# Optimization experiments

Hardware: AMD Instinct MI355X
Metric: run time of the kernel (lower is better)

Reference implementation:

```python
import jax, jax.numpy as jnp
import numpy as np

MODEL_DIM = 1024
NUM_HEADS = 16
HEAD_DIM = MODEL_DIM // NUM_HEADS
B, T = 4, 2048


def setup_inputs() -> dict:
    key = jax.random.key(0)
    ks = jax.random.split(key, 11)
    s = 1.0 / np.sqrt(MODEL_DIM)  # torch Linear default-ish init scale
    def lin(kw, kb):
        W = jax.random.uniform(kw, (MODEL_DIM, MODEL_DIM), jnp.float32, -s, s)
        b = jax.random.uniform(kb, (MODEL_DIM,), jnp.float32, -s, s)
        return W, b
    Wq, bq = lin(ks[0], ks[1])
    Wk, bk = lin(ks[2], ks[3])
    Wv, bv = lin(ks[4], ks[5])
    Wo, bo = lin(ks[6], ks[7])
    query = jax.random.normal(ks[8], (B, T, MODEL_DIM), jnp.float32)
    key_t = jax.random.normal(ks[9], (B, T, MODEL_DIM), jnp.float32)
    value = jax.random.normal(ks[10], (B, T, MODEL_DIM), jnp.float32)
    return {"query": query, "key": key_t, "value": value,
            "Wq": Wq, "bq": bq, "Wk": Wk, "bk": bk,
            "Wv": Wv, "bv": bv, "Wo": Wo, "bo": bo}


def reference(query, key, value, Wq, bq, Wk, bk, Wv, bv, Wo, bo):
    b, tq, d = query.shape
    tk = key.shape[-2]
    h, hd = NUM_HEADS, HEAD_DIM
    # projections; split last dim into heads (torch split/cat == reshape to [b,t,h,hd])
    q = (query @ Wq.T + bq).reshape(b, tq, h, hd)
    k = (key @ Wk.T + bk).reshape(b, tk, h, hd)
    v = (value @ Wv.T + bv).reshape(b, tk, h, hd)
    score = jnp.einsum('bqhd,bkhd->bhqk', q, k) / np.sqrt(hd).astype(np.float32)
    causal = jnp.tril(jnp.ones((tq, tk), dtype=bool))  # mask=True path
    score = jnp.where(causal, score, -jnp.inf)
    probs = jax.nn.softmax(score, axis=-1)
    out = jnp.einsum('bhqk,bkhd->bqhd', probs, v).reshape(b, tq, d)
    return out @ Wo.T + bo
```

## Files before the change

### kernel.cpp

```cpp
#include <hip/hip_runtime.h>
#include <stdint.h>

#define T_SEQ 2048
#define NB    4
#define NH    16
#define DH    64
#define DM    1024
#define MTOT  (NB * T_SEQ)

typedef __attribute__((ext_vector_type(8)))  short  short8;
typedef __attribute__((ext_vector_type(8)))  __bf16 bf16x8;
typedef __attribute__((ext_vector_type(4)))  float  f32x4;
typedef __attribute__((ext_vector_type(16))) float  f32x16;
typedef __attribute__((ext_vector_type(4)))  unsigned short ushort4v;
typedef __attribute__((ext_vector_type(4)))  unsigned int   uint4v;
typedef unsigned short ushort;
typedef unsigned long long u64;

__device__ __forceinline__ ushort f2bf(float x) {
    unsigned int u = __builtin_bit_cast(unsigned int, x);
    u += 0x7FFFu + ((u >> 16) & 1u);
    return (ushort)(u >> 16);
}

__device__ __forceinline__ unsigned cvtpk(float lo, float hi) {
    unsigned r;
    asm("v_cvt_pk_bf16_f32 %0, %1, %2" : "=v"(r) : "v"(lo), "v"(hi));
    return r;
}

__device__ __forceinline__ f32x4 mfma16(short8 a, short8 b, f32x4 c) {
    return __builtin_amdgcn_mfma_f32_16x16x32_bf16(
        __builtin_bit_cast(bf16x8, a), __builtin_bit_cast(bf16x8, b), c, 0, 0, 0);
}
__device__ __forceinline__ f32x16 mfma32(short8 a, short8 b, f32x16 c) {
    return __builtin_amdgcn_mfma_f32_32x32x16_bf16(
        __builtin_bit_cast(bf16x8, a), __builtin_bit_cast(bf16x8, b), c, 0, 0, 0);
}

#define GLOBAL_AS(p) ((const __attribute__((address_space(1))) void*)(p))
#define LDS_AS(p)    ((__attribute__((address_space(3))) void*)(p))

__global__ void cvt4_kernel(const float* __restrict__ s0, const float* __restrict__ s1,
                            const float* __restrict__ s2, const float* __restrict__ s3,
                            ushort* __restrict__ dst) {
    int i = blockIdx.x * 256 + threadIdx.x;
    int which = i >> 18;
    int loc   = i & 262143;
    const float* s = which == 0 ? s0 : which == 1 ? s1 : which == 2 ? s2 : s3;
    f32x4 v = ((const f32x4*)s)[loc];
    ushort4v r;
    r[0] = f2bf(v[0]); r[1] = f2bf(v[1]); r[2] = f2bf(v[2]); r[3] = f2bf(v[3]);
    ((ushort4v*)dst)[i] = r;
}

__global__ __launch_bounds__(256, 4)
void proj_gemm(const float* __restrict__ Xq, const float* __restrict__ Xk,
               const float* __restrict__ Xv, const ushort* __restrict__ Wall,
               const float* __restrict__ bq, const float* __restrict__ bk,
               const float* __restrict__ bv, ushort* __restrict__ P0,
               ushort* __restrict__ Vt, float qscale)
{
    __shared__ __align__(16) ushort sA[128 * 64];
    __shared__ __align__(16) ushort sB[128 * 64];

    const int which = blockIdx.x >> 9;
    const int inner = blockIdx.x & 511;
    const float* X     = which == 0 ? Xq : which == 1 ? Xk : Xv;
    const ushort* Wb   = Wall + (size_t)which * DM * DM;
    const float* bias  = which == 0 ? bq : which == 1 ? bk : bv;

    const int tid  = threadIdx.x;
    const int lane = tid & 63;
    const int w    = tid >> 6;
    const int wr   = (w >> 1) * 64;
    const int wc   = (w & 1) * 64;
    const int bm   = (inner & 63) * 128;
    const int bn   = (inner >> 6) * 128;
    const int lr   = lane & 15;
    const int lk   = lane >> 4;
    const int ofs0 = w * 1024 + lane * 16;

    f32x4 areg[8];
    auto LOAD_A = [&](int kt) {
        #pragma unroll
        for (int i = 0; i < 4; ++i) {
            int ofs  = i * 4096 + ofs0;
            int row  = ofs >> 7;
            int colB = ofs & 127;
            const float* src = X + (size_t)(bm + row) * DM + kt + (colB >> 1);
            areg[2 * i]     = *(const f32x4*)(src);
            areg[2 * i + 1] = *(const f32x4*)(src + 4);
        }
    };
    auto WRITE_A = [&]() {
        #pragma unroll
        for (int i = 0; i < 4; ++i) {
            int ofs  = i * 4096 + ofs0;
            int row  = ofs >> 7;
            int colB = ofs & 127;
            f32x4 v0 = areg[2 * i], v1 = areg[2 * i + 1];
            bf16x8 pk;
            pk[0] = (__bf16)v0[0]; pk[1] = (__bf16)v0[1];
            pk[2] = (__bf16)v0[2]; pk[3] = (__bf16)v0[3];
            pk[4] = (__bf16)v1[0]; pk[5] = (__bf16)v1[1];
            pk[6] = (__bf16)v1[2]; pk[7] = (__bf16)v1[3];
            *(bf16x8*)((char*)sA + row * 128 + (colB ^ ((row & 7) << 4))) = pk;
        }
    };
    auto STAGE_B = [&](int kt) {
        #pragma unroll
        for (int i = 0; i < 4; ++i) {
            int ofs  = i * 4096 + ofs0;
            int row  = ofs >> 7;
            int colB = (ofs & 127) ^ ((row & 7) << 4);
            __builtin_amdgcn_global_load_lds(
                GLOBAL_AS((const char*)Wb + ((size_t)(bn + row) * DM + kt) * 2 + colB),
                LDS_AS((char*)sB + i * 4096 + ofs0), 16, 0, 0);
        }
    };

    f32x4 acc[4][4] = {};
    LOAD_A(0);

    for (int t = 0; t < 16; ++t) {
        __syncthreads();
        WRITE_A();
        STAGE_B(t * 64);
        __syncthreads();
        if (t < 15) LOAD_A((t + 1) * 64);

        #pragma unroll
        for (int kk = 0; kk < 2; ++kk) {
            short8 af[4], bfr[4];
            #pragma unroll
            for (int m = 0; m < 4; ++m) {
                int row = wr + m * 16 + lr;
                int cB  = (kk * 64 + lk * 16) ^ ((row & 7) << 4);
                af[m] = *(const short8*)((const char*)sA + row * 128 + cB);
            }
            #pragma unroll
            for (int n = 0; n < 4; ++n) {
                int row = wc + n * 16 + lr;
                int cB  = (kk * 64 + lk * 16) ^ ((row & 7) << 4);
                bfr[n] = *(const short8*)((const char*)sB + row * 128 + cB);
            }
            #pragma unroll
            for (int m = 0; m < 4; ++m)
                #pragma unroll
                for (int n = 0; n < 4; ++n)
                    acc[m][n] = mfma16(af[m], bfr[n], acc[m][n]);
        }
    }

    const float scale = (which == 0) ? qscale : 1.0f;
    #pragma unroll
    for (int m = 0; m < 4; ++m) {
        #pragma unroll
        for (int n = 0; n < 4; ++n) {
            int col  = bn + wc + n * 16 + lr;
            float bv = bias[col];
            if (which == 2) {
                int row0 = bm + wr + m * 16 + lk * 4;
                int b = row0 >> 11, t0 = row0 & (T_SEQ - 1);
                int h = col >> 6,  d = col & 63;
                int t0p = (t0 & ~12) | ((t0 & 4) << 1) | ((t0 & 8) >> 1);
                u64 pk = 0;
                #pragma unroll
                for (int j = 0; j < 4; ++j)
                    pk |= (u64)f2bf(acc[m][n][j] + bv) << (16 * j);
                *(u64*)(Vt + ((size_t)((b * NH + h) * DH + d)) * T_SEQ + t0p) = pk;
            } else {
                ushort* outp = P0 + (size_t)which * MTOT * DM;
                #pragma unroll
                for (int j = 0; j < 4; ++j) {
                    int row   = bm + wr + m * 16 + lk * 4 + j;
                    float val = (acc[m][n][j] + bv) * scale;
                    int b = row >> 11, t = row & (T_SEQ - 1);
                    int h = col >> 6,  d = col & 63;
                    outp[((size_t)((b * NH + h) * T_SEQ + t)) * DH + d] = f2bf(val);
                }
            }
        }
    }
}

__global__ __launch_bounds__(256, 4)
void out_gemm(const ushort* __restrict__ X, const ushort* __restrict__ Wb,
              const float* __restrict__ bias, float* __restrict__ out)
{
    __shared__ __align__(16) ushort sA[128 * 64];
    __shared__ __align__(16) ushort sB[128 * 64];

    const int tid  = threadIdx.x;
    const int lane = tid & 63;
    const int w    = tid >> 6;
    const int wr   = (w >> 1) * 64;
    const int wc   = (w & 1) * 64;
    const int bm   = (blockIdx.x & 63) * 128;
    const int bn   = (blockIdx.x >> 6) * 128;
    const int lr   = lane & 15;
    const int lk   = lane >> 4;
    const int ofs0 = w * 1024 + lane * 16;

    auto STAGE = [&](const ushort* src0, ushort* dst, int kt) {
        #pragma unroll
        for (int i = 0; i < 4; ++i) {
            int ofs  = i * 4096 + ofs0;
            int row  = ofs >> 7;
            int colB = (ofs & 127) ^ ((row & 7) << 4);
            __builtin_amdgcn_global_load_lds(
                GLOBAL_AS((const char*)src0 + ((size_t)row * DM + kt) * 2 + colB),
                LDS_AS((char*)dst + i * 4096 + ofs0), 16, 0, 0);
        }
    };

    f32x4 acc[4][4] = {};

    for (int t = 0; t < 16; ++t) {
        __syncthreads();
        STAGE(X + (size_t)bm * DM, sA, t * 64);
        STAGE(Wb + (size_t)bn * DM, sB, t * 64);
        __syncthreads();

        #pragma unroll
        for (int kk = 0; kk < 2; ++kk) {
            short8 af[4], bfr[4];
            #pragma unroll
            for (int m = 0; m < 4; ++m) {
                int row = wr + m * 16 + lr;
                int cB  = (kk * 64 + lk * 16) ^ ((row & 7) << 4);
                af[m] = *(const short8*)((const char*)sA + row * 128 + cB);
            }
            #pragma unroll
            for (int n = 0; n < 4; ++n) {
                int row = wc + n * 16 + lr;
                int cB  = (kk * 64 + lk * 16) ^ ((row & 7) << 4);
                bfr[n] = *(const short8*)((const char*)sB + row * 128 + cB);
            }
            #pragma unroll
            for (int m = 0; m < 4; ++m)
                #pragma unroll
                for (int n = 0; n < 4; ++n)
                    acc[m][n] = mfma16(af[m], bfr[n], acc[m][n]);
        }
    }

    #pragma unroll
    for (int m = 0; m < 4; ++m) {
        #pragma unroll
        for (int n = 0; n < 4; ++n) {
            int col  = bn + wc + n * 16 + lr;
            float bv = bias[col];
            #pragma unroll
            for (int j = 0; j < 4; ++j) {
                int row = bm + wr + m * 16 + lk * 4 + j;
                out[(size_t)row * DM + col] = acc[m][n][j] + bv;
            }
        }
    }
}

__global__ __launch_bounds__(256, 4)
void attn_kernel(const ushort* __restrict__ Q, const ushort* __restrict__ K,
                 const ushort* __restrict__ Vt, ushort* __restrict__ O)
{
    __shared__ __align__(16) ushort sK[2][64 * 64];
    __shared__ __align__(16) ushort sV[2][64 * 64];

    const int tid  = threadIdx.x;
    const int lane = tid & 63;
    const int w    = tid >> 6;
    const int l31  = lane & 31;
    const int hi   = lane >> 5;

    const int bh  = blockIdx.x & 63;
    const int g   = blockIdx.x >> 6;
    const int cls = g & 3, pos = g >> 2;
    const int qt  = (pos & 1) ? (4 * cls + (pos >> 1)) : (15 - 4 * cls - (pos >> 1));
    const int b   = bh >> 4, h = bh & 15;

    const ushort* Qbh = Q + (size_t)bh * T_SEQ * DH;
    const char*   Kc  = (const char*)(K  + (size_t)bh * T_SEQ * DH);
    const char*   Vc  = (const char*)(Vt + (size_t)bh * DH * T_SEQ);

    const int scolB = (tid & 7) * 16;
    const int srow  = tid >> 3;

    auto STAGE = [&](int kv, int buf) {
        #pragma unroll
        for (int i = 0; i < 2; ++i) {
            int row = i * 32 + srow;
            int cB  = scolB ^ ((row & 7) << 4);
            __builtin_amdgcn_global_load_lds(
                GLOBAL_AS(Kc + (size_t)(kv * 64 + row) * 128 + cB),
                LDS_AS((char*)&sK[buf][0] + i * 4096 + tid * 16), 16, 0, 0);
        }
        #pragma unroll
        for (int i = 0; i < 2; ++i) {
            int row = i * 32 + srow;
            int cB  = scolB ^ ((row & 7) << 4);
            __builtin_amdgcn_global_load_lds(
                GLOBAL_AS(Vc + (size_t)row * (T_SEQ * 2) + kv * 128 + cB),
                LDS_AS((char*)&sV[buf][0] + i * 4096 + tid * 16), 16, 0, 0);
        }
    };

    const int q0w   = qt * 128 + w * 32;
    const int kvmax = 2 * qt + 1;

    short8 qf[4];
    #pragma unroll
    for (int dc = 0; dc < 4; ++dc)
        qf[dc] = *(const short8*)(Qbh + (size_t)(q0w + l31) * DH + dc * 16 + hi * 8);

    f32x16 o0 = {}, o1 = {};
    float mrow = -1e30f, lsum = 0.f;

    STAGE(0, 0);

    for (int kv = 0; kv <= kvmax; ++kv) {
        const int cur = kv & 1;
        __syncthreads();
        if (kv < kvmax) STAGE(kv + 1, cur ^ 1);
        if (kv * 64 > q0w + 31) continue;

        const char* sk = (const char*)&sK[cur][0];
        const char* sv = (const char*)&sV[cur][0];

        f32x16 s0 = {}, s1 = {};
        __builtin_amdgcn_s_setprio(1);
        #pragma unroll
        for (int dc = 0; dc < 4; ++dc) {
            int cB  = dc * 32 + hi * 16;
            int swz = (l31 & 7) << 4;
            short8 kf0 = *(const short8*)(sk + l31 * 128 + (cB ^ swz));
            short8 kf1 = *(const short8*)(sk + (32 + l31) * 128 + (cB ^ swz));
            s0 = mfma32(kf0, qf[dc], s0);
            s1 = mfma32(kf1, qf[dc], s1);
        }
        __builtin_amdgcn_s_setprio(0);

        if (kv * 64 + 63 > q0w) {
            int q = q0w + l31;
            #pragma unroll
            for (int r = 0; r < 16; ++r) {
                int kp = kv * 64 + (r & 3) + 8 * (r >> 2) + 4 * hi;
                if (kp > q)      s0[r] = -1e30f;
                if (kp + 32 > q) s1[r] = -1e30f;
            }
        }

        float t16[16];
        #pragma unroll
        for (int r = 0; r < 16; ++r) t16[r] = fmaxf(s0[r], s1[r]);
        #pragma unroll
        for (int r = 0; r < 8; ++r)  t16[r] = fmaxf(t16[r], t16[r + 8]);
        #pragma unroll
        for (int r = 0; r < 4; ++r)  t16[r] = fmaxf(t16[r], t16[r + 4]);
        float pm = fmaxf(fmaxf(t16[0], t16[1]), fmaxf(t16[2], t16[3]));
        pm = fmaxf(pm, __shfl_xor(pm, 32));

        if (__any(pm > mrow + 8.f)) {
            float mn = fmaxf(mrow, pm);
            float al = __builtin_amdgcn_exp2f(mrow - mn);
            mrow = mn;
            lsum *= al;
            #pragma unroll
            for (int r = 0; r < 16; ++r) {
                float aq = __shfl(al, (r & 3) + 8 * (r >> 2) + 4 * hi);
                o0[r] *= aq;
                o1[r] *= aq;
            }
        }

        float rs = 0.f;
        #pragma unroll
        for (int r = 0; r < 16; ++r) { s0[r] = __builtin_amdgcn_exp2f(s0[r] - mrow); rs += s0[r]; }
        #pragma unroll
        for (int r = 0; r < 16; ++r) { s1[r] = __builtin_amdgcn_exp2f(s1[r] - mrow); rs += s1[r]; }
        lsum += rs;

        short8 pa[4];
        #pragma unroll
        for (int seg = 0; seg < 4; ++seg) {
            const f32x16& sp = (seg < 2) ? s0 : s1;
            const int r0 = (seg & 1) * 8;
            uint4v pw;
            pw[0] = cvtpk(sp[r0 + 0], sp[r0 + 1]);
            pw[1] = cvtpk(sp[r0 + 2], sp[r0 + 3]);
            pw[2] = cvtpk(sp[r0 + 4], sp[r0 + 5]);
            pw[3] = cvtpk(sp[r0 + 6], sp[r0 + 7]);
            pa[seg] = __builtin_bit_cast(short8, pw);
        }

        __builtin_amdgcn_s_setprio(1);
        #pragma unroll
        for (int seg = 0; seg < 4; ++seg) {
            int cB = seg * 32 + hi * 16;
            {
                int d = l31;
                short8 vf = *(const short8*)(sv + d * 128 + (cB ^ ((d & 7) << 4)));
                o0 = mfma32(pa[seg], vf, o0);
            }
            {
                int d = 32 + l31;
                short8 vf = *(const short8*)(sv + d * 128 + (cB ^ ((d & 7) << 4)));
                o1 = mfma32(pa[seg], vf, o1);
            }
        }
        __builtin_amdgcn_s_setprio(0);
    }

    lsum += __shfl_xor(lsum, 32);
    float rl = 1.0f / lsum;
    #pragma unroll
    for (int r = 0; r < 16; ++r) {
        int   ql = (r & 3) + 8 * (r >> 2) + 4 * hi;
        float rq = __shfl(rl, ql);
        int   t  = q0w + ql;
        size_t base = ((size_t)(b * T_SEQ) + t) * DM + h * DH;
        O[base + l31]      = f2bf(o0[r] * rq);
        O[base + 32 + l31] = f2bf(o1[r] * rq);
    }
}

extern "C" void kernel_launch(void* const* d_in, const int* in_sizes, int n_in,
                              void* d_out, int out_size, void* d_ws, size_t ws_size,
                              hipStream_t stream)
{
    const float* query = (const float*)d_in[0];
    const float* key_t = (const float*)d_in[1];
    const float* value = (const float*)d_in[2];
    const float* Wq = (const float*)d_in[3];
    const float* bq = (const float*)d_in[4];
    const float* Wk = (const float*)d_in[5];
    const float* bk = (const float*)d_in[6];
    const float* Wv = (const float*)d_in[7];
    const float* bv = (const float*)d_in[8];
    const float* Wo = (const float*)d_in[9];
    const float* bo = (const float*)d_in[10];
    float* out = (float*)d_out;

    char* ws = (char*)d_ws;
    const size_t WSZ = (size_t)DM * DM * 2;
    const size_t PSZ = (size_t)MTOT * DM * 2;
    ushort* Wall = (ushort*)(ws);
    ushort* Wo_b = (ushort*)(ws + 3 * WSZ);
    ushort* Qp   = (ushort*)(ws + 4 * WSZ);
    ushort* Kp   = (ushort*)(ws + 4 * WSZ + PSZ);
    ushort* Vt   = (ushort*)(ws + 4 * WSZ + 2 * PSZ);
    ushort* AO   = (ushort*)(ws + 4 * WSZ + 3 * PSZ);

    cvt4_kernel<<<4096, 256, 0, stream>>>(Wq, Wk, Wv, Wo, Wall);

    proj_gemm<<<1536, 256, 0, stream>>>(query, key_t, value, Wall, bq, bk, bv,
                                        Qp, Vt, 0.18033688011112042f);

    attn_kernel<<<1024, 256, 0, stream>>>(Qp, Kp, Vt, AO);

    out_gemm<<<512, 256, 0, stream>>>(AO, Wo_b, bo, out);
}
```

Measured before the change: 169.1 us.

## Pre-convert activations to bf16 and stage both GEMM operands via direct LDS loads

Adds a single conversion kernel that turns the query/key/value activations and all weights into bf16 in a large workspace. The projection GEMM can then stage both A and B with global_load_lds instead of loading fp32 into registers and converting in-kernel. Both GEMMs also remap block indices so consecutive blocks in each XCD share M-tiles, aiming for better L2 reuse. The cost is an extra full write and read of the bf16 activations, a bigger workspace, and a fallback to the old path if the workspace is too small.

```diff
diff --git a/kernel.cpp b/kernel.cpp
--- a/kernel.cpp
+++ b/kernel.cpp
@@ -54,81 +54,79 @@
     ((ushort4v*)dst)[i] = r;
 }
 
+__global__ void cvt_all_kernel(const float* __restrict__ xq, const float* __restrict__ xk,
+                               const float* __restrict__ xv, const float* __restrict__ w0,
+                               const float* __restrict__ w1, const float* __restrict__ w2,
+                               const float* __restrict__ w3, ushort* __restrict__ dst) {
+    const int XU = 2097152;
+    for (int it = 0; it < 14; ++it) {
+        int i = (it * 2048 + blockIdx.x) * 256 + threadIdx.x;
+        const float* s; int loc;
+        if (i < 3 * XU) {
+            int which = i / XU;
+            loc = i - which * XU;
+            s = which == 0 ? xq : which == 1 ? xk : xv;
+        } else {
+            int j = i - 3 * XU;
+            int which = j >> 18;
+            loc = j & 262143;
+            s = which == 0 ? w0 : which == 1 ? w1 : which == 2 ? w2 : w3;
+        }
+        f32x4 v = ((const f32x4*)s)[loc];
+        ushort4v r;
+        r[0] = f2bf(v[0]); r[1] = f2bf(v[1]); r[2] = f2bf(v[2]); r[3] = f2bf(v[3]);
+        ((ushort4v*)dst)[i] = r;
+    }
+}
+
 __global__ __launch_bounds__(256, 4)
-void proj_gemm(const float* __restrict__ Xq, const float* __restrict__ Xk,
-               const float* __restrict__ Xv, const ushort* __restrict__ Wall,
-               const float* __restrict__ bq, const float* __restrict__ bk,
-               const float* __restrict__ bv, ushort* __restrict__ P0,
-               ushort* __restrict__ Vt, float qscale)
+void proj_gemm_bf(const ushort* __restrict__ Xb, const ushort* __restrict__ Wall,
+                  const float* __restrict__ bq, const float* __restrict__ bk,
+                  const float* __restrict__ bv, ushort* __restrict__ P0,
+                  ushort* __restrict__ Vt, float qscale)
 {
     __shared__ __align__(16) ushort sA[128 * 64];
     __shared__ __align__(16) ushort sB[128 * 64];
 
     const int which = blockIdx.x >> 9;
     const int inner = blockIdx.x & 511;
-    const float* X     = which == 0 ? Xq : which == 1 ? Xk : Xv;
+    const int xcd   = inner & 7;
+    const int seq   = inner >> 3;
+    const int bm    = (((seq >> 3) * 8) + xcd) * 128;
+    const int bn    = (seq & 7) * 128;
+
+    const ushort* X    = Xb   + (size_t)which * MTOT * DM;
     const ushort* Wb   = Wall + (size_t)which * DM * DM;
-    const float* bias  = which == 0 ? bq : which == 1 ? bk : bv;
+    const float*  bias = which == 0 ? bq : which == 1 ? bk : bv;
 
     const int tid  = threadIdx.x;
     const int lane = tid & 63;
     const int w    = tid >> 6;
     const int wr   = (w >> 1) * 64;
     const int wc   = (w & 1) * 64;
-    const int bm   = (inner & 63) * 128;
-    const int bn   = (inner >> 6) * 128;
     const int lr   = lane & 15;
     const int lk   = lane >> 4;
     const int ofs0 = w * 1024 + lane * 16;
 
-    f32x4 areg[8];
-    auto LOAD_A = [&](int kt) {
-        #pragma unroll
-        for (int i = 0; i < 4; ++i) {
-            int ofs  = i * 4096 + ofs0;
-            int row  = ofs >> 7;
-            int colB = ofs & 127;
-            const float* src = X + (size_t)(bm + row) * DM + kt + (colB >> 1);
-            areg[2 * i]     = *(const f32x4*)(src);
-            areg[2 * i + 1] = *(const f32x4*)(src + 4);
-        }
-    };
-    auto WRITE_A = [&]() {
-        #pragma unroll
-        for (int i = 0; i < 4; ++i) {
-            int ofs  = i * 4096 + ofs0;
-            int row  = ofs >> 7;
-            int colB = ofs & 127;
-            f32x4 v0 = areg[2 * i], v1 = areg[2 * i + 1];
-            bf16x8 pk;
-            pk[0] = (__bf16)v0[0]; pk[1] = (__bf16)v0[1];
-            pk[2] = (__bf16)v0[2]; pk[3] = (__bf16)v0[3];
-            pk[4] = (__bf16)v1[0]; pk[5] = (__bf16)v1[1];
-            pk[6] = (__bf16)v1[2]; pk[7] = (__bf16)v1[3];
-            *(bf16x8*)((char*)sA + row * 128 + (colB ^ ((row & 7) << 4))) = pk;
-        }
-    };
-    auto STAGE_B = [&](int kt) {
+    auto STAGE = [&](const ushort* src0, ushort* dst, int kt) {
         #pragma unroll
         for (int i = 0; i < 4; ++i) {
             int ofs  = i * 4096 + ofs0;
             int row  = ofs >> 7;
             int colB = (ofs & 127) ^ ((row & 7) << 4);
             __builtin_amdgcn_global_load_lds(
-                GLOBAL_AS((const char*)Wb + ((size_t)(bn + row) * DM + kt) * 2 + colB),
-                LDS_AS((char*)sB + i * 4096 + ofs0), 16, 0, 0);
+                GLOBAL_AS((const char*)src0 + ((size_t)row * DM + kt) * 2 + colB),
+                LDS_AS((char*)dst + i * 4096 + ofs0), 16, 0, 0);
         }
     };
 
     f32x4 acc[4][4] = {};
-    LOAD_A(0);
 
     for (int t = 0; t < 16; ++t) {
         __syncthreads();
-        WRITE_A();
-        STAGE_B(t * 64);
+        STAGE(X + (size_t)bm * DM, sA, t * 64);
+        STAGE(Wb + (size_t)bn * DM, sB, t * 64);
         __syncthreads();
-        if (t < 15) LOAD_A((t + 1) * 64);
 
         #pragma unroll
         for (int kk = 0; kk < 2; ++kk) {
@@ -186,6 +184,137 @@
 }
 
 __global__ __launch_bounds__(256, 4)
+void proj_gemm(const float* __restrict__ Xq, const float* __restrict__ Xk,
+               const float* __restrict__ Xv, const ushort* __restrict__ Wall,
+               const float* __restrict__ bq, const float* __restrict__ bk,
+               const float* __restrict__ bv, ushort* __restrict__ P0,
+               ushort* __restrict__ Vt, float qscale)
+{
+    __shared__ __align__(16) ushort sA[128 * 64];
+    __shared__ __align__(16) ushort sB[128 * 64];
+
+    const int which = blockIdx.x >> 9;
+    const int inner = blockIdx.x & 511;
+    const float* X     = which == 0 ? Xq : which == 1 ? Xk : Xv;
+    const ushort* Wb   = Wall + (size_t)which * DM * DM;
+    const float* bias  = which == 0 ? bq : which == 1 ? bk : bv;
+
+    const int tid  = threadIdx.x;
+    const int lane = tid & 63;
+    const int w    = tid >> 6;
+    const int wr   = (w >> 1) * 64;
+    const int wc   = (w & 1) * 64;
+    const int bm   = (inner & 63) * 128;
+    const int bn   = (inner >> 6) * 128;
+    const int lr   = lane & 15;
+    const int lk   = lane >> 4;
+    const int ofs0 = w * 1024 + lane * 16;
+
+    f32x4 areg[8];
+    auto LOAD_A = [&](int kt) {
+        #pragma unroll
+        for (int i = 0; i < 4; ++i) {
+            int ofs  = i * 4096 + ofs0;
+            int row  = ofs >> 7;
+            int colB = ofs & 127;
+            const float* src = X + (size_t)(bm + row) * DM + kt + (colB >> 1);
+            areg[2 * i]     = *(const f32x4*)(src);
+            areg[2 * i + 1] = *(const f32x4*)(src + 4);
+        }
+    };
+    auto WRITE_A = [&]() {
+        #pragma unroll
+        for (int i = 0; i < 4; ++i) {
+            int ofs  = i * 4096 + ofs0;
+            int row  = ofs >> 7;
+            int colB = ofs & 127;
+            f32x4 v0 = areg[2 * i], v1 = areg[2 * i + 1];
+            bf16x8 pk;
+            pk[0] = (__bf16)v0[0]; pk[1] = (__bf16)v0[1];
+            pk[2] = (__bf16)v0[2]; pk[3] = (__bf16)v0[3];
+            pk[4] = (__bf16)v1[0]; pk[5] = (__bf16)v1[1];
+            pk[6] = (__bf16)v1[2]; pk[7] = (__bf16)v1[3];
+            *(bf16x8*)((char*)sA + row * 128 + (colB ^ ((row & 7) << 4))) = pk;
+        }
+    };
+    auto STAGE_B = [&](int kt) {
+        #pragma unroll
+        for (int i = 0; i < 4; ++i) {
+            int ofs  = i * 4096 + ofs0;
+            int row  = ofs >> 7;
+            int colB = (ofs & 127) ^ ((row & 7) << 4);
+            __builtin_amdgcn_global_load_lds(
+                GLOBAL_AS((const char*)Wb + ((size_t)(bn + row) * DM + kt) * 2 + colB),
+                LDS_AS((char*)sB + i * 4096 + ofs0), 16, 0, 0);
+        }
+    };
+
+    f32x4 acc[4][4] = {};
+    LOAD_A(0);
+
+    for (int t = 0; t < 16; ++t) {
+        __syncthreads();
+        WRITE_A();
+        STAGE_B(t * 64);
+        __syncthreads();
+        if (t < 15) LOAD_A((t + 1) * 64);
+
+        #pragma unroll
+        for (int kk = 0; kk < 2; ++kk) {
+            short8 af[4], bfr[4];
+            #pragma unroll
+            for (int m = 0; m < 4; ++m) {
+                int row = wr + m * 16 + lr;
+                int cB  = (kk * 64 + lk * 16) ^ ((row & 7) << 4);
+                af[m] = *(const short8*)((const char*)sA + row * 128 + cB);
+            }
+            #pragma unroll
+            for (int n = 0; n < 4; ++n) {
+                int row = wc + n * 16 + lr;
+                int cB  = (kk * 64 + lk * 16) ^ ((row & 7) << 4);
+                bfr[n] = *(const short8*)((const char*)sB + row * 128 + cB);
+            }
+            #pragma unroll
+            for (int m = 0; m < 4; ++m)
+                #pragma unroll
+                for (int n = 0; n < 4; ++n)
+                    acc[m][n] = mfma16(af[m], bfr[n], acc[m][n]);
+        }
+    }
+
+    const float scale = (which == 0) ? qscale : 1.0f;
+    #pragma unroll
+    for (int m = 0; m < 4; ++m) {
+        #pragma unroll
+        for (int n = 0; n < 4; ++n) {
+            int col  = bn + wc + n * 16 + lr;
+            float bv = bias[col];
+            if (which == 2) {
+                int row0 = bm + wr + m * 16 + lk * 4;
+                int b = row0 >> 11, t0 = row0 & (T_SEQ - 1);
+                int h = col >> 6,  d = col & 63;
+                int t0p = (t0 & ~12) | ((t0 & 4) << 1) | ((t0 & 8) >> 1);
+                u64 pk = 0;
+                #pragma unroll
+                for (int j = 0; j < 4; ++j)
+                    pk |= (u64)f2bf(acc[m][n][j] + bv) << (16 * j);
+                *(u64*)(Vt + ((size_t)((b * NH + h) * DH + d)) * T_SEQ + t0p) = pk;
+            } else {
+                ushort* outp = P0 + (size_t)which * MTOT * DM;
+                #pragma unroll
+                for (int j = 0; j < 4; ++j) {
+                    int row   = bm + wr + m * 16 + lk * 4 + j;
+                    float val = (acc[m][n][j] + bv) * scale;
+                    int b = row >> 11, t = row & (T_SEQ - 1);
+                    int h = col >> 6,  d = col & 63;
+                    outp[((size_t)((b * NH + h) * T_SEQ + t)) * DH + d] = f2bf(val);
+                }
+            }
+        }
+    }
+}
+
+__global__ __launch_bounds__(256, 4)
 void out_gemm(const ushort* __restrict__ X, const ushort* __restrict__ Wb,
               const float* __restrict__ bias, float* __restrict__ out)
 {
@@ -197,8 +326,10 @@
     const int w    = tid >> 6;
     const int wr   = (w >> 1) * 64;
     const int wc   = (w & 1) * 64;
-    const int bm   = (blockIdx.x & 63) * 128;
-    const int bn   = (blockIdx.x >> 6) * 128;
+    const int xcd  = blockIdx.x & 7;
+    const int seq  = blockIdx.x >> 3;
+    const int bm   = (((seq >> 3) * 8) + xcd) * 128;
+    const int bn   = (seq & 7) * 128;
     const int lr   = lane & 15;
     const int lk   = lane >> 4;
     const int ofs0 = w * 1024 + lane * 16;
@@ -445,19 +576,35 @@
     char* ws = (char*)d_ws;
     const size_t WSZ = (size_t)DM * DM * 2;
     const size_t PSZ = (size_t)MTOT * DM * 2;
-    ushort* Wall = (ushort*)(ws);
-    ushort* Wo_b = (ushort*)(ws + 3 * WSZ);
-    ushort* Qp   = (ushort*)(ws + 4 * WSZ);
-    ushort* Kp   = (ushort*)(ws + 4 * WSZ + PSZ);
-    ushort* Vt   = (ushort*)(ws + 4 * WSZ + 2 * PSZ);
-    ushort* AO   = (ushort*)(ws + 4 * WSZ + 3 * PSZ);
-
-    cvt4_kernel<<<4096, 256, 0, stream>>>(Wq, Wk, Wv, Wo, Wall);
-
-    proj_gemm<<<1536, 256, 0, stream>>>(query, key_t, value, Wall, bq, bk, bv,
-                                        Qp, Vt, 0.18033688011112042f);
-
-    attn_kernel<<<1024, 256, 0, stream>>>(Qp, Kp, Vt, AO);
-
-    out_gemm<<<512, 256, 0, stream>>>(AO, Wo_b, bo, out);
-}
+    const float QSCALE = 0.18033688011112042f;
+
+    const size_t NEED_BIG = 3 * PSZ + 4 * WSZ + 3 * PSZ;
+
+    if (ws_size >= NEED_BIG) {
+        ushort* Xb   = (ushort*)(ws);
+        ushort* Wall = (ushort*)(ws + 3 * PSZ);
+        ushort* Wo_b = (ushort*)(ws + 3 * PSZ + 3 * WSZ);
+        ushort* Qp   = (ushort*)(ws + 3 * PSZ + 4 * WSZ);
+        ushort* Kp   = Qp + MTOT * DM;
+        ushort* Vt   = Kp + MTOT * DM;
+        ushort* AO   = Xb;
+
+        cvt_all_kernel<<<2048, 256, 0, stream>>>(query, key_t, value, Wq, Wk, Wv, Wo, Xb);
+        proj_gemm_bf<<<1536, 256, 0, stream>>>(Xb, Wall, bq, bk, bv, Qp, Vt, QSCALE);
+        attn_kernel<<<1024, 256, 0, stream>>>(Qp, Kp, Vt, AO);
+        out_gemm<<<512, 256, 0, stream>>>(AO, Wo_b, bo, out);
+    } else {
+        ushort* Wall = (ushort*)(ws);
+        ushort* Wo_b = (ushort*)(ws + 3 * WSZ);
+        ushort* Qp   = (ushort*)(ws + 4 * WSZ);
+        ushort* Kp   = (ushort*)(ws + 4 * WSZ + PSZ);
+        ushort* Vt   = (ushort*)(ws + 4 * WSZ + 2 * PSZ);
+        ushort* AO   = (ushort*)(ws + 4 * WSZ + 3 * PSZ);
+
+        cvt4_kernel<<<4096, 256, 0, stream>>>(Wq, Wk, Wv, Wo, Wall);
+        proj_gemm<<<1536, 256, 0, stream>>>(query, key_t, value, Wall, bq, bk, bv,
+                                            Qp, Vt, QSCALE);
+        attn_kernel<<<1024, 256, 0, stream>>>(Qp, Kp, Vt, AO);
+        out_gemm<<<512, 256, 0, stream>>>(AO, Wo_b, bo, out);
+    }
+}
```

Measured after the change: 161.8 us. -4.3%, faster.
